# Kernel tuning notes

Measured on AMD Instinct MI355X. Metric: run time of the kernel, lower is better.

Reference implementation:

```python
import jax, jax.numpy as jnp
import numpy as np

B, K = 2048, 128
M = 5 * K
ALPHA = 1.0 / K          # alpha_k = 1/K
VARTHETA = 0.1
PMAX = 10.0
BIG = 1e9


def _gnn(HW, X, W0a, W1a, W0b, W1b):
    """Order-1 graph filter GNN (HWGCN, K0=[1,1]): relu hidden layer, linear output.
    HW: (B,K,K), X: (B,K,Fin) -> (B,K,Fout)."""
    SX = jnp.einsum('bij,bjf->bif', HW, X)
    Z = jax.nn.relu(X @ W0a + SX @ W1a)              # (B,K,32)
    SZ = jnp.einsum('bij,bjh->bih', HW, Z)
    return Z @ W0b + SZ @ W1b                        # (B,K,Fout)


def setup_inputs() -> dict:
    key = jax.random.key(0)
    ks = jax.random.split(key, 16)
    s = 0.05
    d = {
        'num_itr': 10,
        'kth': 9,
        'HW': jnp.abs(jax.random.normal(ks[0], (B, K, K), jnp.float32)) * s,
        'x0_tmp': jax.random.uniform(ks[1], (B, M), jnp.float32),
        'nu3_val': jnp.array([0.1], jnp.float32),
        'tilde_gamma_val': jnp.array([2.0], jnp.float32),
        'A9': jax.random.normal(ks[2], (1,), jnp.float32),
        'A1': jax.random.normal(ks[3], (1,), jnp.float32),
        'A3': jax.random.normal(ks[4], (1,), jnp.float32),
        'A7': jax.random.normal(ks[5], (1,), jnp.float32),
        'b7': jax.random.normal(ks[6], (1,), jnp.float32),
        'A10': jax.random.normal(ks[7], (1,), jnp.float32),
        'g1_W0a': jax.random.normal(ks[8], (5, 32), jnp.float32) * s,
        'g1_W1a': jax.random.normal(ks[9], (5, 32), jnp.float32) * s,
        'g1_W0b': jax.random.normal(ks[10], (32, 2), jnp.float32) * s,
        'g1_W1b': jax.random.normal(ks[11], (32, 2), jnp.float32) * s,
        'g2_W0a': jax.random.normal(ks[12], (K + 5, 32), jnp.float32) * s,
        'g2_W1a': jax.random.normal(ks[13], (K + 5, 32), jnp.float32) * s,
        'g2_W0b': jax.random.normal(ks[14], (32, 5), jnp.float32) * s,
        'g2_W1b': jax.random.normal(ks[15], (32, 5), jnp.float32) * s,
    }
    return d


def reference(num_itr, kth, HW, x0_tmp, nu3_val, tilde_gamma_val,
              A9, A1, A3, A7, b7, A10,
              g1_W0a, g1_W1a, g1_W0b, g1_W1b,
              g2_W0a, g2_W1a, g2_W0b, g2_W1b):
    nu3 = nu3_val[0]
    tg = tilde_gamma_val[0]
    x = x0_tmp                                        # (B, 5K)

    # REGNN 1 -> step sizes lbd (B,2)
    X1 = x.reshape(B, 5, K).transpose(0, 2, 1)        # (B,K,5)
    lbd = jax.nn.relu(jnp.mean(_gnn(HW, X1, g1_W0a, g1_W1a, g1_W0b, g1_W1b), axis=1))

    # vectorized per-K gradient steps on segments [K:2K] and [4K:5K]
    s0, s1, s2, s3, s4 = (x[:, i * K:(i + 1) * K] for i in range(5))
    s1 = s1 - lbd[:, 0:1] * (ALPHA / (1.0 + s1))
    s4 = s4 + lbd[:, 1:2] * (ALPHA * VARTHETA)
    x = jnp.concatenate([s0, s1, s2, s3, s4], axis=1)

    # REGNN 2 correction
    X2 = x.reshape(B, 5, K).transpose(0, 2, 1)        # (B,K,5)
    tilde = _gnn(HW, jnp.concatenate([HW, X2], axis=-1),
                 g2_W0a, g2_W1a, g2_W0b, g2_W1b)      # (B,K,5)
    x = x + tilde.transpose(0, 2, 1).reshape(B, M)

    # proj onto C8: sum of first K entries <= Pmax (||q||^2 = K)
    f = jnp.sum(x[:, :K], axis=1) - PMAX              # (B,)
    q = jnp.concatenate([jnp.ones(K, x.dtype), jnp.zeros(4 * K, x.dtype)])
    x = jnp.where((f <= 0)[:, None], x, x - f[:, None] * q / K)

    # banded elementwise box clamps (faithful sequential max/min)
    idx = jnp.arange(M)
    band = lambda a, b: (idx >= a) & (idx < b)
    Vnu = 1.0 - 1.0 / (1.0 + nu3) ** 2
    Vg = 1.0 - 1.0 / (1.0 + tg) ** 2
    x = jnp.maximum(jnp.where(band(K, 2 * K), nu3, 0.0), x)
    x = jnp.minimum(jnp.where(band(2 * K, 3 * K), tg, BIG), x)
    x = jnp.maximum(jnp.where(band(3 * K, 4 * K), Vnu, 0.0), x)
    x = jnp.minimum(jnp.where(band(3 * K, 4 * K), Vg, BIG), x)

    if kth == num_itr - 1:  # static python branch
        x = jnp.maximum(x, 0.0)
        xg = x[:, 2 * K:3 * K]   # gamma
        xv = x[:, 3 * K:4 * K]   # V
        f5 = 1.0 - 1.0 / (1.0 + xg) ** 2 - xv
        f6 = jnp.sqrt(xv) - x[:, 4 * K:5 * K]
        p = x[:, 0:K]
        nu = x[:, K:2 * K]
        diagHW = jnp.diagonal(HW, axis1=1, axis2=2)   # (B,K)
        top = p * diagHW
        down = jnp.einsum('bi,bij->bj', p, HW) - top + 1.0
        f4 = top - down * xg
        f2 = nu * down - top
        return (x, f5, f6, f4, f2)
    return (x,)
```

## Files before the change

kernel.cpp:

```cpp
#include <hip/hip_runtime.h>
#include <math.h>

#define B_N 2048
#define KK 128
#define MM 640
#define HS 136
#define ZS 40
#define ALPHA (1.0f/128.0f)
#define VARTHETA 0.1f
#define PMAXV 10.0f
#define BIGV 1000000000.0f

typedef __attribute__((ext_vector_type(8))) short short8;
typedef __attribute__((ext_vector_type(4))) float floatx4;

static __device__ __forceinline__ unsigned short f2bf(float f) {
    unsigned u = __builtin_bit_cast(unsigned, f);
    u += 0x7fffu + ((u >> 16) & 1u);
    return (unsigned short)(u >> 16);
}
static __device__ __forceinline__ float bf2f(unsigned short h) {
    unsigned u = ((unsigned)h) << 16;
    return __builtin_bit_cast(float, u);
}

__global__ __launch_bounds__(512, 4)
void unfold_pocs_kernel(
    const int* __restrict__ num_itr_p, const int* __restrict__ kth_p,
    const float* __restrict__ HW, const float* __restrict__ x0,
    const float* __restrict__ nu3_p, const float* __restrict__ tg_p,
    const float* __restrict__ g1_W0a, const float* __restrict__ g1_W1a,
    const float* __restrict__ g1_W0b, const float* __restrict__ g1_W1b,
    const float* __restrict__ g2_W0a, const float* __restrict__ g2_W1a,
    const float* __restrict__ g2_W0b, const float* __restrict__ g2_W1b,
    float* __restrict__ out)
{
    __shared__ __align__(16) unsigned short hwb[KK*HS];
    __shared__ __align__(16) unsigned short w1aT[32*HS];
    __shared__ __align__(16) unsigned short c2T[32*HS];
    __shared__ __align__(16) unsigned short zb[KK*ZS];
    __shared__ __align__(16) unsigned short eT[5*HS];
    __shared__ __align__(16) float scr8[KK*8];
    __shared__ __align__(16) float xb[MM];
    __shared__ __align__(16) float g1w0a[160], g1w1a[160];
    __shared__ __align__(16) float g1w0b[64],  g1w1b[64];
    __shared__ __align__(16) float w0a2b[160], w1a2b[160];
    __shared__ __align__(16) float w0b2[160],  w1b2[160];
    __shared__ float red[16];
    __shared__ float lbd_l[2];
    __shared__ float fval_l;

    const int t = threadIdx.x;
    const int b = blockIdx.x;
    const float* HWb = HW + (size_t)b * (KK*KK);

    #pragma unroll
    for (int it = 0; it < 8; ++it) {
        int qi = it * 512 + t;
        int row = qi >> 5, q = qi & 31;
        float4 v = *(const float4*)(HWb + row*KK + q*4);
        ushort4 p4;
        p4.x = f2bf(v.x); p4.y = f2bf(v.y); p4.z = f2bf(v.z); p4.w = f2bf(v.w);
        *(ushort4*)&hwb[row*HS + q*4] = p4;
    }
    #pragma unroll
    for (int it = 0; it < 8; ++it) {
        int idx = it * 512 + t;
        int k = idx >> 5, n = idx & 31;
        w1aT[n*HS + k] = f2bf(g2_W1a[k*32 + n]);
    }
    if (t < 160) {
        *(float4*)(xb + t*4) = *(const float4*)(x0 + (size_t)b*MM + t*4);
        g1w0a[t] = g1_W0a[t];
        g1w1a[t] = g1_W1a[t];
        w0a2b[t] = g2_W0a[KK*32 + t];
        w1a2b[t] = g2_W1a[KK*32 + t];
        w0b2[t]  = g2_W0b[t];
        w1b2[t]  = g2_W1b[t];
    }
    if (t < 64) { g1w0b[t] = g1_W0b[t]; g1w1b[t] = g1_W1b[t]; }
    __syncthreads();

    const int wv = t >> 6, lane = t & 63, quad = lane >> 4, lr = lane & 15;

    {
        floatx4 acc = {0.f, 0.f, 0.f, 0.f};
        const int ns = lr < 5 ? lr : 4;
        #pragma unroll
        for (int kt = 0; kt < 4; ++kt) {
            short8 a = *(const short8*)&hwb[(wv*16 + lr)*HS + kt*32 + quad*8];
            float4 f0 = *(const float4*)(xb + ns*KK + kt*32 + quad*8);
            float4 f1 = *(const float4*)(xb + ns*KK + kt*32 + quad*8 + 4);
            short8 bb;
            bb[0]=(short)f2bf(f0.x); bb[1]=(short)f2bf(f0.y); bb[2]=(short)f2bf(f0.z); bb[3]=(short)f2bf(f0.w);
            bb[4]=(short)f2bf(f1.x); bb[5]=(short)f2bf(f1.y); bb[6]=(short)f2bf(f1.z); bb[7]=(short)f2bf(f1.w);
            acc = __builtin_amdgcn_mfma_f32_16x16x32_bf16(a, bb, acc, 0, 0, 0);
        }
        if (lr < 5) {
            #pragma unroll
            for (int r = 0; r < 4; ++r)
                scr8[(wv*16 + quad*4 + r)*8 + lr] = acc[r];
        }
    }
    __syncthreads();

    const int row = t >> 2, g = t & 3;

    {
        float sx[5], x1r[5];
        #pragma unroll
        for (int f = 0; f < 5; ++f) { sx[f] = scr8[row*8 + f]; x1r[f] = xb[f*KK + row]; }

        float zb0p0=0, zb0p1=0, zb1p0=0, zb1p1=0;
        #pragma unroll
        for (int hh = 0; hh < 8; ++hh) {
            int h = 8*g + hh;
            float a = 0.0f;
            #pragma unroll
            for (int f = 0; f < 5; ++f) a += x1r[f]*g1w0a[f*32+h] + sx[f]*g1w1a[f*32+h];
            a = fmaxf(a, 0.0f);
            zb0p0 += a * g1w0b[h*2+0];
            zb0p1 += a * g1w0b[h*2+1];
            zb1p0 += a * g1w1b[h*2+0];
            zb1p1 += a * g1w1b[h*2+1];
        }
        float mp = 0.0f;
        for (int w = 0; w < 32; ++w) {
            int i = 4*w + g;
            mp += bf2f(hwb[i*HS + row]);
        }
        mp += __shfl_xor(mp, 1); mp += __shfl_xor(mp, 2);
        float m = mp * (1.0f/KK);
        float c0 = zb0p0*(1.0f/KK) + m*zb1p0;
        float c1 = zb0p1*(1.0f/KK) + m*zb1p1;
        #pragma unroll
        for (int s = 1; s < 64; s <<= 1) { c0 += __shfl_xor(c0, s); c1 += __shfl_xor(c1, s); }
        if ((t & 63) == 0) { red[(t>>6)*2] = c0; red[(t>>6)*2 + 1] = c1; }
    }
    __syncthreads();
    if (t == 0) {
        float a0=0, a1=0;
        for (int w2 = 0; w2 < 8; ++w2) { a0 += red[w2*2]; a1 += red[w2*2+1]; }
        lbd_l[0] = fmaxf(a0, 0.0f);
        lbd_l[1] = fmaxf(a1, 0.0f);
    }
    __syncthreads();

    if (t < KK) {
        float s1v = xb[KK + t];
        xb[KK + t]   = s1v - lbd_l[0] * (ALPHA / (1.0f + s1v));
        xb[4*KK + t] += lbd_l[1] * (ALPHA * VARTHETA);
    }
    __syncthreads();

    short8 A[4];
    #pragma unroll
    for (int kt = 0; kt < 4; ++kt)
        A[kt] = *(const short8*)&hwb[(wv*16 + lr)*HS + kt*32 + quad*8];

    #pragma unroll
    for (int nt = 0; nt < 2; ++nt) {
        floatx4 acc = {0.f, 0.f, 0.f, 0.f};
        #pragma unroll
        for (int kt = 0; kt < 4; ++kt) {
            short8 bb = *(const short8*)&w1aT[(nt*16 + lr)*HS + kt*32 + quad*8];
            acc = __builtin_amdgcn_mfma_f32_16x16x32_bf16(A[kt], bb, acc, 0, 0, 0);
        }
        const int n = nt*16 + lr;
        ushort4 p4;
        unsigned short pe[4];
        #pragma unroll
        for (int r = 0; r < 4; ++r) {
            int mm = wv*16 + quad*4 + r;
            float v = acc[r] + g2_W0a[mm*32 + n];
            #pragma unroll
            for (int f = 0; f < 5; ++f) v += xb[f*KK + mm] * w1a2b[f*32 + n];
            pe[r] = f2bf(v);
        }
        p4.x = pe[0]; p4.y = pe[1]; p4.z = pe[2]; p4.w = pe[3];
        *(ushort4*)&c2T[n*HS + wv*16 + quad*4] = p4;
    }
    __syncthreads();

    #pragma unroll
    for (int nt = 0; nt < 2; ++nt) {
        floatx4 acc = {0.f, 0.f, 0.f, 0.f};
        #pragma unroll
        for (int kt = 0; kt < 4; ++kt) {
            short8 bb = *(const short8*)&c2T[(nt*16 + lr)*HS + kt*32 + quad*8];
            acc = __builtin_amdgcn_mfma_f32_16x16x32_bf16(A[kt], bb, acc, 0, 0, 0);
        }
        const int n = nt*16 + lr;
        #pragma unroll
        for (int r = 0; r < 4; ++r) {
            int mm = wv*16 + quad*4 + r;
            float v = acc[r];
            #pragma unroll
            for (int f = 0; f < 5; ++f) v += xb[f*KK + mm] * w0a2b[f*32 + n];
            zb[mm*ZS + n] = f2bf(fmaxf(v, 0.0f));
        }
    }
    __syncthreads();

    {
        float ev[5] = {0,0,0,0,0}, t0v[5] = {0,0,0,0,0};
        #pragma unroll
        for (int hh = 0; hh < 8; ++hh) {
            int h = 8*g + hh;
            float zv = bf2f(zb[row*ZS + h]);
            #pragma unroll
            for (int c = 0; c < 5; ++c) {
                ev[c]  += zv * w1b2[h*5 + c];
                t0v[c] += zv * w0b2[h*5 + c];
            }
        }
        #pragma unroll
        for (int c = 0; c < 5; ++c) {
            ev[c]  += __shfl_xor(ev[c], 1);  ev[c]  += __shfl_xor(ev[c], 2);
            t0v[c] += __shfl_xor(t0v[c], 1); t0v[c] += __shfl_xor(t0v[c], 2);
        }
        if (g == 0) {
            #pragma unroll
            for (int c = 0; c < 5; ++c) {
                eT[c*HS + row] = f2bf(ev[c]);
                scr8[row*8 + c] = t0v[c];
            }
        }
    }
    __syncthreads();

    {
        floatx4 acc = {0.f, 0.f, 0.f, 0.f};
        const int ns = lr < 5 ? lr : 4;
        #pragma unroll
        for (int kt = 0; kt < 4; ++kt) {
            short8 bb = *(const short8*)&eT[ns*HS + kt*32 + quad*8];
            acc = __builtin_amdgcn_mfma_f32_16x16x32_bf16(A[kt], bb, acc, 0, 0, 0);
        }
        if (lr < 5) {
            #pragma unroll
            for (int r = 0; r < 4; ++r) {
                int mm = wv*16 + quad*4 + r;
                xb[lr*KK + mm] += acc[r] + scr8[mm*8 + lr];
            }
        }
    }
    __syncthreads();

    float pv = (t < KK) ? xb[t] : 0.0f;
    #pragma unroll
    for (int s = 1; s < 64; s <<= 1) pv += __shfl_xor(pv, s);
    if ((t & 63) == 0) red[t >> 6] = pv;
    __syncthreads();
    if (t == 0) {
        float fs = 0.0f;
        for (int w2 = 0; w2 < 8; ++w2) fs += red[w2];
        fval_l = fs - PMAXV;
    }
    __syncthreads();

    const int num_itr = num_itr_p[0], kth = kth_p[0];
    const bool flag = (kth == num_itr - 1);
    const float nu3 = nu3_p[0], tg = tg_p[0];
    const float onu = 1.0f + nu3, otg = 1.0f + tg;
    const float Vnu = 1.0f - 1.0f/(onu*onu), Vg = 1.0f - 1.0f/(otg*otg);
    const float fv = fval_l;
    float* outx = out + (size_t)b * MM;

    #pragma unroll
    for (int r2 = 0; r2 < 2; ++r2) {
        int idx = r2*512 + t;
        if (idx < MM) {
            float v = xb[idx];
            if (idx < KK && fv > 0.0f) v -= fv * (1.0f/KK);
            v = fmaxf(v, (idx >= KK   && idx < 2*KK) ? nu3 : 0.0f);
            v = fminf(v, (idx >= 2*KK && idx < 3*KK) ? tg  : BIGV);
            v = fmaxf(v, (idx >= 3*KK && idx < 4*KK) ? Vnu : 0.0f);
            v = fminf(v, (idx >= 3*KK && idx < 4*KK) ? Vg  : BIGV);
            if (flag) v = fmaxf(v, 0.0f);
            xb[idx] = v;
            outx[idx] = v;
        }
    }
    __syncthreads();

    if (flag) {
        const size_t O1 = (size_t)B_N*MM;
        const size_t OK = (size_t)B_N*KK;
        if (t < KK) {
            float xg = xb[2*KK + t], xv = xb[3*KK + t];
            float u1 = 1.0f + xg;
            out[O1 + (size_t)b*KK + t]      = 1.0f - 1.0f/(u1*u1) - xv;
            out[O1 + OK + (size_t)b*KK + t] = sqrtf(xv) - xb[4*KK + t];
        }
        float dp = 0.0f;
        for (int w = 0; w < 32; ++w) {
            int i = 4*w + g;
            dp += xb[i] * bf2f(hwb[i*HS + row]);
        }
        dp += __shfl_xor(dp, 1); dp += __shfl_xor(dp, 2);
        if (g == 0) {
            float p = xb[row], nuv = xb[KK + row], xg = xb[2*KK + row];
            float diag = bf2f(hwb[row*HS + row]);
            float top = p * diag;
            float down = dp - top + 1.0f;
            out[O1 + 2*OK + (size_t)b*KK + row] = top - down * xg;
            out[O1 + 3*OK + (size_t)b*KK + row] = nuv * down - top;
        }
    }
}

extern "C" void kernel_launch(void* const* d_in, const int* in_sizes, int n_in,
                              void* d_out, int out_size, void* d_ws, size_t ws_size,
                              hipStream_t stream) {
    unfold_pocs_kernel<<<dim3(B_N), dim3(512), 0, stream>>>(
        (const int*)d_in[0], (const int*)d_in[1],
        (const float*)d_in[2], (const float*)d_in[3],
        (const float*)d_in[4], (const float*)d_in[5],
        (const float*)d_in[12], (const float*)d_in[13],
        (const float*)d_in[14], (const float*)d_in[15],
        (const float*)d_in[16], (const float*)d_in[17],
        (const float*)d_in[18], (const float*)d_in[19],
        (float*)d_out);
}
```

Before: 258.6 us.

## Keep HW tile in registers, drop LDS copy and alias scratch buffers

Each lane now loads its MFMA A-fragment of HW straight from global memory into registers and never stages the whole bf16 HW matrix in LDS. Column sums and the final p·HW reductions become shuffle reductions over those register fragments. The remaining scratch buffers share one aliased pool, which cuts LDS per block so launch bounds can rise from 4 to 6 blocks per CU. Several barriers and single-thread reduction steps are folded away. In exchange there are more shuffle reductions, the aliasing needs extra barriers inside the loops, and register pressure is higher.

```diff
diff --git a/kernel.cpp b/kernel.cpp
--- a/kernel.cpp
+++ b/kernel.cpp
@@ -5,7 +5,7 @@
 #define KK 128
 #define MM 640
 #define HS 136
-#define ZS 40
+#define ZSS 40
 #define ALPHA (1.0f/128.0f)
 #define VARTHETA 0.1f
 #define PMAXV 10.0f
@@ -24,7 +24,11 @@
     return __builtin_bit_cast(float, u);
 }
 
-__global__ __launch_bounds__(512, 4)
+#define POOLA_OFF 0
+#define POOLB_OFF 10240
+#define POOL_BYTES (10240 + 8704)
+
+__global__ __launch_bounds__(512, 6)
 void unfold_pocs_kernel(
     const int* __restrict__ num_itr_p, const int* __restrict__ kth_p,
     const float* __restrict__ HW, const float* __restrict__ x0,
@@ -35,39 +39,46 @@
     const float* __restrict__ g2_W0b, const float* __restrict__ g2_W1b,
     float* __restrict__ out)
 {
-    __shared__ __align__(16) unsigned short hwb[KK*HS];
-    __shared__ __align__(16) unsigned short w1aT[32*HS];
-    __shared__ __align__(16) unsigned short c2T[32*HS];
-    __shared__ __align__(16) unsigned short zb[KK*ZS];
-    __shared__ __align__(16) unsigned short eT[5*HS];
+    __shared__ __align__(16) unsigned char pool[POOL_BYTES];
+    __shared__ __align__(16) float xb[MM];
     __shared__ __align__(16) float scr8[KK*8];
-    __shared__ __align__(16) float xb[MM];
     __shared__ __align__(16) float g1w0a[160], g1w1a[160];
     __shared__ __align__(16) float g1w0b[64],  g1w1b[64];
     __shared__ __align__(16) float w0a2b[160], w1a2b[160];
     __shared__ __align__(16) float w0b2[160],  w1b2[160];
     __shared__ float red[16];
-    __shared__ float lbd_l[2];
-    __shared__ float fval_l;
+
+    unsigned short* w1aT  = (unsigned short*)(pool + POOLA_OFF);
+    unsigned short* zbp   = (unsigned short*)(pool + POOLA_OFF);
+    float*          colred= (float*)(pool + POOLB_OFF);
+    unsigned short* c2T   = (unsigned short*)(pool + POOLB_OFF);
+    unsigned short* eT    = (unsigned short*)(pool + POOLB_OFF);
+    float*          dpred = (float*)(pool + POOLB_OFF + 2048);
+    float*          diagl = (float*)(pool + POOLB_OFF + 6400);
 
     const int t = threadIdx.x;
     const int b = blockIdx.x;
     const float* HWb = HW + (size_t)b * (KK*KK);
 
-    #pragma unroll
-    for (int it = 0; it < 8; ++it) {
-        int qi = it * 512 + t;
-        int row = qi >> 5, q = qi & 31;
-        float4 v = *(const float4*)(HWb + row*KK + q*4);
-        ushort4 p4;
-        p4.x = f2bf(v.x); p4.y = f2bf(v.y); p4.z = f2bf(v.z); p4.w = f2bf(v.w);
-        *(ushort4*)&hwb[row*HS + q*4] = p4;
-    }
-    #pragma unroll
-    for (int it = 0; it < 8; ++it) {
-        int idx = it * 512 + t;
-        int k = idx >> 5, n = idx & 31;
-        w1aT[n*HS + k] = f2bf(g2_W1a[k*32 + n]);
+    const int wv = t >> 6, lane = t & 63, quad = lane >> 4, lr = lane & 15;
+    const int arow = wv*16 + lr;
+
+    short8 A[4];
+    #pragma unroll
+    for (int kt = 0; kt < 4; ++kt) {
+        float4 f0 = *(const float4*)(HWb + arow*KK + kt*32 + quad*8);
+        float4 f1 = *(const float4*)(HWb + arow*KK + kt*32 + quad*8 + 4);
+        short8 a;
+        a[0]=(short)f2bf(f0.x); a[1]=(short)f2bf(f0.y); a[2]=(short)f2bf(f0.z); a[3]=(short)f2bf(f0.w);
+        a[4]=(short)f2bf(f1.x); a[5]=(short)f2bf(f1.y); a[6]=(short)f2bf(f1.z); a[7]=(short)f2bf(f1.w);
+        A[kt] = a;
+    }
+    {
+        const int n = t & 31, seg = t >> 5;
+        unsigned short tmp[8];
+        #pragma unroll
+        for (int i = 0; i < 8; ++i) tmp[i] = f2bf(g2_W1a[(seg*8 + i)*32 + n]);
+        *(short8*)&w1aT[n*HS + seg*8] = *(short8*)tmp;
     }
     if (t < 160) {
         *(float4*)(xb + t*4) = *(const float4*)(x0 + (size_t)b*MM + t*4);
@@ -81,25 +92,37 @@
     if (t < 64) { g1w0b[t] = g1_W0b[t]; g1w1b[t] = g1_W1b[t]; }
     __syncthreads();
 
-    const int wv = t >> 6, lane = t & 63, quad = lane >> 4, lr = lane & 15;
-
     {
         floatx4 acc = {0.f, 0.f, 0.f, 0.f};
         const int ns = lr < 5 ? lr : 4;
         #pragma unroll
         for (int kt = 0; kt < 4; ++kt) {
-            short8 a = *(const short8*)&hwb[(wv*16 + lr)*HS + kt*32 + quad*8];
             float4 f0 = *(const float4*)(xb + ns*KK + kt*32 + quad*8);
             float4 f1 = *(const float4*)(xb + ns*KK + kt*32 + quad*8 + 4);
             short8 bb;
             bb[0]=(short)f2bf(f0.x); bb[1]=(short)f2bf(f0.y); bb[2]=(short)f2bf(f0.z); bb[3]=(short)f2bf(f0.w);
             bb[4]=(short)f2bf(f1.x); bb[5]=(short)f2bf(f1.y); bb[6]=(short)f2bf(f1.z); bb[7]=(short)f2bf(f1.w);
-            acc = __builtin_amdgcn_mfma_f32_16x16x32_bf16(a, bb, acc, 0, 0, 0);
+            acc = __builtin_amdgcn_mfma_f32_16x16x32_bf16(A[kt], bb, acc, 0, 0, 0);
         }
         if (lr < 5) {
             #pragma unroll
             for (int r = 0; r < 4; ++r)
                 scr8[(wv*16 + quad*4 + r)*8 + lr] = acc[r];
+        }
+    }
+    #pragma unroll
+    for (int kt = 0; kt < 4; ++kt) {
+        float v[8];
+        #pragma unroll
+        for (int j = 0; j < 8; ++j) v[j] = bf2f((unsigned short)A[kt][j]);
+        #pragma unroll
+        for (int mk = 1; mk < 16; mk <<= 1)
+            #pragma unroll
+            for (int j = 0; j < 8; ++j) v[j] += __shfl_xor(v[j], mk);
+        if (lr == 0) {
+            float4 a0 = {v[0],v[1],v[2],v[3]}, a1 = {v[4],v[5],v[6],v[7]};
+            *(float4*)&colred[wv*128 + kt*32 + quad*8]     = a0;
+            *(float4*)&colred[wv*128 + kt*32 + quad*8 + 4] = a1;
         }
     }
     __syncthreads();
@@ -124,39 +147,29 @@
             zb1p0 += a * g1w1b[h*2+0];
             zb1p1 += a * g1w1b[h*2+1];
         }
-        float mp = 0.0f;
-        for (int w = 0; w < 32; ++w) {
-            int i = 4*w + g;
-            mp += bf2f(hwb[i*HS + row]);
-        }
-        mp += __shfl_xor(mp, 1); mp += __shfl_xor(mp, 2);
-        float m = mp * (1.0f/KK);
+        float msum = colred[(2*g)*128 + row] + colred[(2*g+1)*128 + row];
+        msum += __shfl_xor(msum, 1); msum += __shfl_xor(msum, 2);
+        float m = msum * (1.0f/KK);
         float c0 = zb0p0*(1.0f/KK) + m*zb1p0;
         float c1 = zb0p1*(1.0f/KK) + m*zb1p1;
         #pragma unroll
         for (int s = 1; s < 64; s <<= 1) { c0 += __shfl_xor(c0, s); c1 += __shfl_xor(c1, s); }
-        if ((t & 63) == 0) { red[(t>>6)*2] = c0; red[(t>>6)*2 + 1] = c1; }
-    }
-    __syncthreads();
-    if (t == 0) {
-        float a0=0, a1=0;
-        for (int w2 = 0; w2 < 8; ++w2) { a0 += red[w2*2]; a1 += red[w2*2+1]; }
-        lbd_l[0] = fmaxf(a0, 0.0f);
-        lbd_l[1] = fmaxf(a1, 0.0f);
-    }
-    __syncthreads();
-
-    if (t < KK) {
-        float s1v = xb[KK + t];
-        xb[KK + t]   = s1v - lbd_l[0] * (ALPHA / (1.0f + s1v));
-        xb[4*KK + t] += lbd_l[1] * (ALPHA * VARTHETA);
-    }
-    __syncthreads();
-
-    short8 A[4];
-    #pragma unroll
-    for (int kt = 0; kt < 4; ++kt)
-        A[kt] = *(const short8*)&hwb[(wv*16 + lr)*HS + kt*32 + quad*8];
+        if ((t & 63) == 0) { red[wv*2] = c0; red[wv*2 + 1] = c1; }
+    }
+    __syncthreads();
+
+    {
+        float lbd0 = 0.f, lbd1 = 0.f;
+        #pragma unroll
+        for (int w2 = 0; w2 < 8; ++w2) { lbd0 += red[w2*2]; lbd1 += red[w2*2+1]; }
+        lbd0 = fmaxf(lbd0, 0.0f); lbd1 = fmaxf(lbd1, 0.0f);
+        if (t < KK) {
+            float s1v = xb[KK + t];
+            xb[KK + t]   = s1v - lbd0 * (ALPHA / (1.0f + s1v));
+            xb[4*KK + t] += lbd1 * (ALPHA * VARTHETA);
+        }
+    }
+    __syncthreads();
 
     #pragma unroll
     for (int nt = 0; nt < 2; ++nt) {
@@ -167,7 +180,6 @@
             acc = __builtin_amdgcn_mfma_f32_16x16x32_bf16(A[kt], bb, acc, 0, 0, 0);
         }
         const int n = nt*16 + lr;
-        ushort4 p4;
         unsigned short pe[4];
         #pragma unroll
         for (int r = 0; r < 4; ++r) {
@@ -177,7 +189,8 @@
             for (int f = 0; f < 5; ++f) v += xb[f*KK + mm] * w1a2b[f*32 + n];
             pe[r] = f2bf(v);
         }
-        p4.x = pe[0]; p4.y = pe[1]; p4.z = pe[2]; p4.w = pe[3];
+        if (nt == 0) __syncthreads();
+        ushort4 p4; p4.x = pe[0]; p4.y = pe[1]; p4.z = pe[2]; p4.w = pe[3];
         *(ushort4*)&c2T[n*HS + wv*16 + quad*4] = p4;
     }
     __syncthreads();
@@ -191,23 +204,36 @@
             acc = __builtin_amdgcn_mfma_f32_16x16x32_bf16(A[kt], bb, acc, 0, 0, 0);
         }
         const int n = nt*16 + lr;
-        #pragma unroll
-        for (int r = 0; r < 4; ++r) {
-            int mm = wv*16 + quad*4 + r;
-            float v = acc[r];
-            #pragma unroll
-            for (int f = 0; f < 5; ++f) v += xb[f*KK + mm] * w0a2b[f*32 + n];
-            zb[mm*ZS + n] = f2bf(fmaxf(v, 0.0f));
+        if (nt == 1) {
+            #pragma unroll
+            for (int r = 0; r < 4; ++r) {
+                int mm = wv*16 + quad*4 + r;
+                float v = acc[r];
+                #pragma unroll
+                for (int f = 0; f < 5; ++f) v += xb[f*KK + mm] * w0a2b[f*32 + n];
+                zbp[mm*ZSS + n] = f2bf(fmaxf(v, 0.0f));
+            }
+        } else {
+            __syncthreads();
+            #pragma unroll
+            for (int r = 0; r < 4; ++r) {
+                int mm = wv*16 + quad*4 + r;
+                float v = acc[r];
+                #pragma unroll
+                for (int f = 0; f < 5; ++f) v += xb[f*KK + mm] * w0a2b[f*32 + n];
+                zbp[mm*ZSS + n] = f2bf(fmaxf(v, 0.0f));
+            }
         }
     }
     __syncthreads();
 
     {
         float ev[5] = {0,0,0,0,0}, t0v[5] = {0,0,0,0,0};
+        short8 zrow = *(const short8*)&zbp[row*ZSS + g*8];
         #pragma unroll
         for (int hh = 0; hh < 8; ++hh) {
             int h = 8*g + hh;
-            float zv = bf2f(zb[row*ZS + h]);
+            float zv = bf2f((unsigned short)zrow[hh]);
             #pragma unroll
             for (int c = 0; c < 5; ++c) {
                 ev[c]  += zv * w1b2[h*5 + c];
@@ -222,7 +248,7 @@
         if (g == 0) {
             #pragma unroll
             for (int c = 0; c < 5; ++c) {
-                eT[c*HS + row] = f2bf(ev[c]);
+                eT[c*HS + row]  = f2bf(ev[c]);
                 scr8[row*8 + c] = t0v[c];
             }
         }
@@ -250,21 +276,17 @@
     float pv = (t < KK) ? xb[t] : 0.0f;
     #pragma unroll
     for (int s = 1; s < 64; s <<= 1) pv += __shfl_xor(pv, s);
-    if ((t & 63) == 0) red[t >> 6] = pv;
-    __syncthreads();
-    if (t == 0) {
-        float fs = 0.0f;
-        for (int w2 = 0; w2 < 8; ++w2) fs += red[w2];
-        fval_l = fs - PMAXV;
-    }
-    __syncthreads();
+    if ((t & 63) == 0) red[wv] = pv;
+    __syncthreads();
+    float fv = -PMAXV;
+    #pragma unroll
+    for (int w2 = 0; w2 < 8; ++w2) fv += red[w2];
 
     const int num_itr = num_itr_p[0], kth = kth_p[0];
     const bool flag = (kth == num_itr - 1);
     const float nu3 = nu3_p[0], tg = tg_p[0];
     const float onu = 1.0f + nu3, otg = 1.0f + tg;
     const float Vnu = 1.0f - 1.0f/(onu*onu), Vg = 1.0f - 1.0f/(otg*otg);
-    const float fv = fval_l;
     float* outx = out + (size_t)b * MM;
 
     #pragma unroll
@@ -282,9 +304,9 @@
             outx[idx] = v;
         }
     }
-    __syncthreads();
 
     if (flag) {
+        __syncthreads();
         const size_t O1 = (size_t)B_N*MM;
         const size_t OK = (size_t)B_N*KK;
         if (t < KK) {
@@ -293,19 +315,50 @@
             out[O1 + (size_t)b*KK + t]      = 1.0f - 1.0f/(u1*u1) - xv;
             out[O1 + OK + (size_t)b*KK + t] = sqrtf(xv) - xb[4*KK + t];
         }
-        float dp = 0.0f;
-        for (int w = 0; w < 32; ++w) {
-            int i = 4*w + g;
-            dp += xb[i] * bf2f(hwb[i*HS + row]);
-        }
-        dp += __shfl_xor(dp, 1); dp += __shfl_xor(dp, 2);
-        if (g == 0) {
-            float p = xb[row], nuv = xb[KK + row], xg = xb[2*KK + row];
-            float diag = bf2f(hwb[row*HS + row]);
-            float top = p * diag;
-            float down = dp - top + 1.0f;
-            out[O1 + 2*OK + (size_t)b*KK + row] = top - down * xg;
-            out[O1 + 3*OK + (size_t)b*KK + row] = nuv * down - top;
+        {
+            int kt_n = wv >> 1;
+            int qexp = ((wv & 1) << 1) + (lr >> 3);
+            if (quad == qexp) {
+                short8 av = A[0];
+                if (kt_n == 1) av = A[1];
+                else if (kt_n == 2) av = A[2];
+                else if (kt_n == 3) av = A[3];
+                int j = lr & 7;
+                float dv = 0.f;
+                #pragma unroll
+                for (int jj = 0; jj < 8; ++jj) if (jj == j) dv = bf2f((unsigned short)av[jj]);
+                diagl[arow] = dv;
+            }
+        }
+        {
+            float p = xb[arow];
+            #pragma unroll
+            for (int kt = 0; kt < 4; ++kt) {
+                float v[8];
+                #pragma unroll
+                for (int j = 0; j < 8; ++j) v[j] = p * bf2f((unsigned short)A[kt][j]);
+                #pragma unroll
+                for (int mk = 1; mk < 16; mk <<= 1)
+                    #pragma unroll
+                    for (int j = 0; j < 8; ++j) v[j] += __shfl_xor(v[j], mk);
+                if (lr == 0) {
+                    float4 a0 = {v[0],v[1],v[2],v[3]}, a1 = {v[4],v[5],v[6],v[7]};
+                    *(float4*)&dpred[wv*128 + kt*32 + quad*8]     = a0;
+                    *(float4*)&dpred[wv*128 + kt*32 + quad*8 + 4] = a1;
+                }
+            }
+        }
+        __syncthreads();
+        {
+            float ds = dpred[(2*g)*128 + row] + dpred[(2*g+1)*128 + row];
+            ds += __shfl_xor(ds, 1); ds += __shfl_xor(ds, 2);
+            if (g == 0) {
+                float p_  = xb[row], nuv = xb[KK + row], xg = xb[2*KK + row];
+                float top = p_ * diagl[row];
+                float down = ds - top + 1.0f;
+                out[O1 + 2*OK + (size_t)b*KK + row] = top - down * xg;
+                out[O1 + 3*OK + (size_t)b*KK + row] = nuv * down - top;
+            }
         }
     }
 }
```

Measured after the change: 309.5 us. +19.7%, slower.

## Fold extra 5 features into MFMA, alias LDS buffers, cut redundant syncs

Applied to the files above, without the earlier changes.

The scalar loops over the 5 extra input features in both GNN layer-2 stages are replaced by an additional bf16 MFMA that uses precomputed bf16 copies of x and the weight tails. Several shared buffers now alias one pool to shrink LDS use. The lambda and f reductions are done redundantly by every thread instead of thread 0, which removes barriers, and the final sync is moved inside the flag branch. Conversions use native bf16 vector casts, and the w1a transpose writes vectorised stores. Rounding the 5-feature term to bf16 lowers its precision slightly.

```diff
diff --git a/kernel.cpp b/kernel.cpp
--- a/kernel.cpp
+++ b/kernel.cpp
@@ -5,24 +5,32 @@
 #define KK 128
 #define MM 640
 #define HS 136
-#define ZS 40
+#define ZSS 40
+#define SXS 12
 #define ALPHA (1.0f/128.0f)
 #define VARTHETA 0.1f
 #define PMAXV 10.0f
 #define BIGV 1000000000.0f
 
 typedef __attribute__((ext_vector_type(8))) short short8;
+typedef __attribute__((ext_vector_type(4))) short short4v;
 typedef __attribute__((ext_vector_type(4))) float floatx4;
+typedef __attribute__((ext_vector_type(4))) __bf16 bf16x4;
 
 static __device__ __forceinline__ unsigned short f2bf(float f) {
-    unsigned u = __builtin_bit_cast(unsigned, f);
-    u += 0x7fffu + ((u >> 16) & 1u);
-    return (unsigned short)(u >> 16);
+    return __builtin_bit_cast(unsigned short, (__bf16)f);
+}
+static __device__ __forceinline__ short4v cvt4(floatx4 v) {
+    return __builtin_bit_cast(short4v, __builtin_convertvector(v, bf16x4));
 }
 static __device__ __forceinline__ float bf2f(unsigned short h) {
     unsigned u = ((unsigned)h) << 16;
     return __builtin_bit_cast(float, u);
 }
+
+#define POOLA_OFF 0
+#define POOLB_OFF 10240
+#define POOL_BYTES (10240 + 8704)
 
 __global__ __launch_bounds__(512, 4)
 void unfold_pocs_kernel(
@@ -36,70 +44,75 @@
     float* __restrict__ out)
 {
     __shared__ __align__(16) unsigned short hwb[KK*HS];
-    __shared__ __align__(16) unsigned short w1aT[32*HS];
-    __shared__ __align__(16) unsigned short c2T[32*HS];
-    __shared__ __align__(16) unsigned short zb[KK*ZS];
-    __shared__ __align__(16) unsigned short eT[5*HS];
-    __shared__ __align__(16) float scr8[KK*8];
+    __shared__ __align__(16) unsigned char pool[POOL_BYTES];
     __shared__ __align__(16) float xb[MM];
+    __shared__ __align__(16) unsigned short xbf[5*HS];
+    __shared__ __align__(16) unsigned short x2bf[KK*8];
+    __shared__ __align__(16) unsigned short w1abf[32*8];
+    __shared__ __align__(16) unsigned short w0abf[32*8];
     __shared__ __align__(16) float g1w0a[160], g1w1a[160];
     __shared__ __align__(16) float g1w0b[64],  g1w1b[64];
-    __shared__ __align__(16) float w0a2b[160], w1a2b[160];
     __shared__ __align__(16) float w0b2[160],  w1b2[160];
     __shared__ float red[16];
-    __shared__ float lbd_l[2];
-    __shared__ float fval_l;
+
+    unsigned short* w1aT = (unsigned short*)(pool + POOLA_OFF);
+    unsigned short* zbp  = (unsigned short*)(pool + POOLA_OFF);
+    float*          SXs  = (float*)(pool + POOLB_OFF);
+    unsigned short* c2T  = (unsigned short*)(pool + POOLB_OFF);
+    unsigned short* eT   = (unsigned short*)(pool + POOLB_OFF);
+    float*          t0f  = (float*)(pool + POOLB_OFF + 2048);
 
     const int t = threadIdx.x;
     const int b = blockIdx.x;
     const float* HWb = HW + (size_t)b * (KK*KK);
 
+    const int wv = t >> 6, lane = t & 63, quad = lane >> 4, lr = lane & 15;
+    const int arow = wv*16 + lr;
+
     #pragma unroll
     for (int it = 0; it < 8; ++it) {
         int qi = it * 512 + t;
         int row = qi >> 5, q = qi & 31;
-        float4 v = *(const float4*)(HWb + row*KK + q*4);
-        ushort4 p4;
-        p4.x = f2bf(v.x); p4.y = f2bf(v.y); p4.z = f2bf(v.z); p4.w = f2bf(v.w);
-        *(ushort4*)&hwb[row*HS + q*4] = p4;
-    }
-    #pragma unroll
-    for (int it = 0; it < 8; ++it) {
-        int idx = it * 512 + t;
-        int k = idx >> 5, n = idx & 31;
-        w1aT[n*HS + k] = f2bf(g2_W1a[k*32 + n]);
+        floatx4 v = *(const floatx4*)(HWb + row*KK + q*4);
+        *(short4v*)&hwb[row*HS + q*4] = cvt4(v);
+    }
+    {
+        const int n = t & 31, seg = t >> 5;
+        unsigned short tmp[8];
+        #pragma unroll
+        for (int i = 0; i < 8; ++i) tmp[i] = f2bf(g2_W1a[(seg*8 + i)*32 + n]);
+        *(short8*)&w1aT[n*HS + seg*8] = *(short8*)tmp;
+    }
+    {
+        const int n = (t & 255) >> 3, j = t & 7;
+        if (t < 256) w1abf[t]       = (j < 5) ? f2bf(g2_W1a[(KK + j)*32 + n]) : (unsigned short)0;
+        else if (t < 512) w0abf[t - 256] = (j < 5) ? f2bf(g2_W0a[(KK + j)*32 + n]) : (unsigned short)0;
     }
     if (t < 160) {
-        *(float4*)(xb + t*4) = *(const float4*)(x0 + (size_t)b*MM + t*4);
+        floatx4 v = *(const floatx4*)(x0 + (size_t)b*MM + t*4);
+        *(floatx4*)(xb + t*4) = v;
+        *(short4v*)&xbf[(t >> 5)*HS + ((t*4) & 127)] = cvt4(v);
         g1w0a[t] = g1_W0a[t];
         g1w1a[t] = g1_W1a[t];
-        w0a2b[t] = g2_W0a[KK*32 + t];
-        w1a2b[t] = g2_W1a[KK*32 + t];
         w0b2[t]  = g2_W0b[t];
         w1b2[t]  = g2_W1b[t];
     }
     if (t < 64) { g1w0b[t] = g1_W0b[t]; g1w1b[t] = g1_W1b[t]; }
     __syncthreads();
 
-    const int wv = t >> 6, lane = t & 63, quad = lane >> 4, lr = lane & 15;
-
     {
         floatx4 acc = {0.f, 0.f, 0.f, 0.f};
         const int ns = lr < 5 ? lr : 4;
         #pragma unroll
         for (int kt = 0; kt < 4; ++kt) {
-            short8 a = *(const short8*)&hwb[(wv*16 + lr)*HS + kt*32 + quad*8];
-            float4 f0 = *(const float4*)(xb + ns*KK + kt*32 + quad*8);
-            float4 f1 = *(const float4*)(xb + ns*KK + kt*32 + quad*8 + 4);
-            short8 bb;
-            bb[0]=(short)f2bf(f0.x); bb[1]=(short)f2bf(f0.y); bb[2]=(short)f2bf(f0.z); bb[3]=(short)f2bf(f0.w);
-            bb[4]=(short)f2bf(f1.x); bb[5]=(short)f2bf(f1.y); bb[6]=(short)f2bf(f1.z); bb[7]=(short)f2bf(f1.w);
+            short8 a  = *(const short8*)&hwb[arow*HS + kt*32 + quad*8];
+            short8 bb = *(const short8*)&xbf[ns*HS   + kt*32 + quad*8];
             acc = __builtin_amdgcn_mfma_f32_16x16x32_bf16(a, bb, acc, 0, 0, 0);
         }
         if (lr < 5) {
             #pragma unroll
             for (int r = 0; r < 4; ++r)
-                scr8[(wv*16 + quad*4 + r)*8 + lr] = acc[r];
+                SXs[(wv*16 + quad*4 + r)*SXS + lr] = acc[r];
         }
     }
     __syncthreads();
@@ -109,7 +122,7 @@
     {
         float sx[5], x1r[5];
         #pragma unroll
-        for (int f = 0; f < 5; ++f) { sx[f] = scr8[row*8 + f]; x1r[f] = xb[f*KK + row]; }
+        for (int f = 0; f < 5; ++f) { sx[f] = SXs[row*SXS + f]; x1r[f] = xb[f*KK + row]; }
 
         float zb0p0=0, zb0p1=0, zb1p0=0, zb1p1=0;
         #pragma unroll
@@ -135,79 +148,83 @@
         float c1 = zb0p1*(1.0f/KK) + m*zb1p1;
         #pragma unroll
         for (int s = 1; s < 64; s <<= 1) { c0 += __shfl_xor(c0, s); c1 += __shfl_xor(c1, s); }
-        if ((t & 63) == 0) { red[(t>>6)*2] = c0; red[(t>>6)*2 + 1] = c1; }
-    }
-    __syncthreads();
-    if (t == 0) {
-        float a0=0, a1=0;
-        for (int w2 = 0; w2 < 8; ++w2) { a0 += red[w2*2]; a1 += red[w2*2+1]; }
-        lbd_l[0] = fmaxf(a0, 0.0f);
-        lbd_l[1] = fmaxf(a1, 0.0f);
-    }
-    __syncthreads();
-
-    if (t < KK) {
-        float s1v = xb[KK + t];
-        xb[KK + t]   = s1v - lbd_l[0] * (ALPHA / (1.0f + s1v));
-        xb[4*KK + t] += lbd_l[1] * (ALPHA * VARTHETA);
+        if (lane == 0) { red[wv*2] = c0; red[wv*2 + 1] = c1; }
+    }
+    __syncthreads();
+
+    {
+        float lbd0 = 0.f, lbd1 = 0.f;
+        #pragma unroll
+        for (int w2 = 0; w2 < 8; ++w2) { lbd0 += red[w2*2]; lbd1 += red[w2*2+1]; }
+        lbd0 = fmaxf(lbd0, 0.0f); lbd1 = fmaxf(lbd1, 0.0f);
+
+        const int i0 = 2*t, m = i0 >> 3, f0 = i0 & 7;
+        float va = (f0     < 5) ? xb[f0*KK + m]     : 0.f;
+        float vb = (f0 + 1 < 5) ? xb[(f0+1)*KK + m] : 0.f;
+        if (f0 == 0) { vb = vb - lbd0 * (ALPHA / (1.0f + vb)); xb[KK + m]   = vb; }
+        if (f0 == 4) { va = va + lbd1 * (ALPHA * VARTHETA);    xb[4*KK + m] = va; }
+        ushort2 p; p.x = f2bf(va); p.y = f2bf(vb);
+        *(ushort2*)&x2bf[i0] = p;
     }
     __syncthreads();
 
     short8 A[4];
     #pragma unroll
     for (int kt = 0; kt < 4; ++kt)
-        A[kt] = *(const short8*)&hwb[(wv*16 + lr)*HS + kt*32 + quad*8];
+        A[kt] = *(const short8*)&hwb[arow*HS + kt*32 + quad*8];
 
     #pragma unroll
     for (int nt = 0; nt < 2; ++nt) {
+        const int n = nt*16 + lr, mmb = wv*16 + quad*4;
         floatx4 acc = {0.f, 0.f, 0.f, 0.f};
+        short8 ax2 = {0,0,0,0,0,0,0,0}, bx2 = {0,0,0,0,0,0,0,0};
+        if (quad == 0) {
+            ax2 = *(const short8*)&x2bf[(wv*16 + lr)*8];
+            bx2 = *(const short8*)&w1abf[n*8];
+        }
+        acc = __builtin_amdgcn_mfma_f32_16x16x32_bf16(ax2, bx2, acc, 0, 0, 0);
         #pragma unroll
         for (int kt = 0; kt < 4; ++kt) {
-            short8 bb = *(const short8*)&w1aT[(nt*16 + lr)*HS + kt*32 + quad*8];
+            short8 bb = *(const short8*)&w1aT[n*HS + kt*32 + quad*8];
             acc = __builtin_amdgcn_mfma_f32_16x16x32_bf16(A[kt], bb, acc, 0, 0, 0);
         }
-        const int n = nt*16 + lr;
-        ushort4 p4;
-        unsigned short pe[4];
-        #pragma unroll
-        for (int r = 0; r < 4; ++r) {
-            int mm = wv*16 + quad*4 + r;
-            float v = acc[r] + g2_W0a[mm*32 + n];
-            #pragma unroll
-            for (int f = 0; f < 5; ++f) v += xb[f*KK + mm] * w1a2b[f*32 + n];
-            pe[r] = f2bf(v);
-        }
-        p4.x = pe[0]; p4.y = pe[1]; p4.z = pe[2]; p4.w = pe[3];
-        *(ushort4*)&c2T[n*HS + wv*16 + quad*4] = p4;
+        ushort4 pe;
+        pe.x = f2bf(acc[0] + g2_W0a[(mmb+0)*32 + n]);
+        pe.y = f2bf(acc[1] + g2_W0a[(mmb+1)*32 + n]);
+        pe.z = f2bf(acc[2] + g2_W0a[(mmb+2)*32 + n]);
+        pe.w = f2bf(acc[3] + g2_W0a[(mmb+3)*32 + n]);
+        *(ushort4*)&c2T[n*HS + mmb] = pe;
     }
     __syncthreads();
 
     #pragma unroll
     for (int nt = 0; nt < 2; ++nt) {
+        const int n = nt*16 + lr, mmb = wv*16 + quad*4;
         floatx4 acc = {0.f, 0.f, 0.f, 0.f};
+        short8 ax2 = {0,0,0,0,0,0,0,0}, bx2 = {0,0,0,0,0,0,0,0};
+        if (quad == 0) {
+            ax2 = *(const short8*)&x2bf[(wv*16 + lr)*8];
+            bx2 = *(const short8*)&w0abf[n*8];
+        }
+        acc = __builtin_amdgcn_mfma_f32_16x16x32_bf16(ax2, bx2, acc, 0, 0, 0);
         #pragma unroll
         for (int kt = 0; kt < 4; ++kt) {
-            short8 bb = *(const short8*)&c2T[(nt*16 + lr)*HS + kt*32 + quad*8];
+            short8 bb = *(const short8*)&c2T[n*HS + kt*32 + quad*8];
             acc = __builtin_amdgcn_mfma_f32_16x16x32_bf16(A[kt], bb, acc, 0, 0, 0);
         }
-        const int n = nt*16 + lr;
-        #pragma unroll
-        for (int r = 0; r < 4; ++r) {
-            int mm = wv*16 + quad*4 + r;
-            float v = acc[r];
-            #pragma unroll
-            for (int f = 0; f < 5; ++f) v += xb[f*KK + mm] * w0a2b[f*32 + n];
-            zb[mm*ZS + n] = f2bf(fmaxf(v, 0.0f));
-        }
+        #pragma unroll
+        for (int r = 0; r < 4; ++r)
+            zbp[(mmb + r)*ZSS + n] = f2bf(fmaxf(acc[r], 0.0f));
     }
     __syncthreads();
 
     {
         float ev[5] = {0,0,0,0,0}, t0v[5] = {0,0,0,0,0};
+        short8 zrow = *(const short8*)&zbp[row*ZSS + g*8];
         #pragma unroll
         for (int hh = 0; hh < 8; ++hh) {
             int h = 8*g + hh;
-            float zv = bf2f(zb[row*ZS + h]);
+            float zv = bf2f((unsigned short)zrow[hh]);
             #pragma unroll
             for (int c = 0; c < 5; ++c) {
                 ev[c]  += zv * w1b2[h*5 + c];
@@ -222,8 +239,8 @@
         if (g == 0) {
             #pragma unroll
             for (int c = 0; c < 5; ++c) {
-                eT[c*HS + row] = f2bf(ev[c]);
-                scr8[row*8 + c] = t0v[c];
+                eT[c*HS + row]  = f2bf(ev[c]);
+                t0f[row*8 + c]  = t0v[c];
             }
         }
     }
@@ -241,7 +258,7 @@
             #pragma unroll
             for (int r = 0; r < 4; ++r) {
                 int mm = wv*16 + quad*4 + r;
-                xb[lr*KK + mm] += acc[r] + scr8[mm*8 + lr];
+                xb[lr*KK + mm] += acc[r] + t0f[mm*8 + lr];
             }
         }
     }
@@ -250,21 +267,17 @@
     float pv = (t < KK) ? xb[t] : 0.0f;
     #pragma unroll
     for (int s = 1; s < 64; s <<= 1) pv += __shfl_xor(pv, s);
-    if ((t & 63) == 0) red[t >> 6] = pv;
-    __syncthreads();
-    if (t == 0) {
-        float fs = 0.0f;
-        for (int w2 = 0; w2 < 8; ++w2) fs += red[w2];
-        fval_l = fs - PMAXV;
-    }
-    __syncthreads();
+    if (lane == 0) red[wv] = pv;
+    __syncthreads();
+    float fv = -PMAXV;
+    #pragma unroll
+    for (int w2 = 0; w2 < 8; ++w2) fv += red[w2];
 
     const int num_itr = num_itr_p[0], kth = kth_p[0];
     const bool flag = (kth == num_itr - 1);
     const float nu3 = nu3_p[0], tg = tg_p[0];
     const float onu = 1.0f + nu3, otg = 1.0f + tg;
     const float Vnu = 1.0f - 1.0f/(onu*onu), Vg = 1.0f - 1.0f/(otg*otg);
-    const float fv = fval_l;
     float* outx = out + (size_t)b * MM;
 
     #pragma unroll
@@ -282,9 +295,9 @@
             outx[idx] = v;
         }
     }
-    __syncthreads();
 
     if (flag) {
+        __syncthreads();
         const size_t O1 = (size_t)B_N*MM;
         const size_t OK = (size_t)B_N*KK;
         if (t < KK) {
@@ -300,9 +313,9 @@
         }
         dp += __shfl_xor(dp, 1); dp += __shfl_xor(dp, 2);
         if (g == 0) {
-            float p = xb[row], nuv = xb[KK + row], xg = xb[2*KK + row];
+            float p_  = xb[row], nuv = xb[KK + row], xg = xb[2*KK + row];
             float diag = bf2f(hwb[row*HS + row]);
-            float top = p * diag;
+            float top  = p_ * diag;
             float down = dp - top + 1.0f;
             out[O1 + 2*OK + (size_t)b*KK + row] = top - down * xg;
             out[O1 + 3*OK + (size_t)b*KK + row] = nuv * down - top;
```

Result: faster. 252.8 us (-2.2%).
